# Optimization experiments

Hardware: AMD Instinct MI355X
Metric: run time of the kernel (lower is better)

## Reference

```python
import jax, jax.numpy as jnp
import numpy as np

B, X, T = 4, 128, 256
PARAM_DIM, HIDDEN, EMB, DH, LATENT = 16, 128, 128, 32, 32


def _w(key, fan_in, fan_out):
    return jax.random.normal(key, (fan_in, fan_out), dtype=jnp.float32) / np.sqrt(fan_in)


def setup_inputs() -> dict:
    key = jax.random.key(0)
    ks = jax.random.split(key, 32)
    d = {
        "x": jax.random.normal(ks[0], (B, X, 1), dtype=jnp.float32),
        "t": jax.random.normal(ks[1], (B, T, 1), dtype=jnp.float32),
        "param": jax.random.normal(ks[2], (B, PARAM_DIM), dtype=jnp.float32),
        # p2e: SymmetricInitDNN([param_dim, hidden, emb], 'sin')
        "p2e_W1": _w(ks[3], PARAM_DIM, HIDDEN), "p2e_b1": jnp.zeros((HIDDEN,), jnp.float32),
        "p2e_W2": _w(ks[4], HIDDEN, EMB), "p2e_b2": jnp.zeros((EMB,), jnp.float32),
        "e2ex_W": _w(ks[5], EMB, EMB), "e2ex_b": jnp.zeros((EMB,), jnp.float32),
        "e2et_W": _w(ks[6], EMB, EMB), "e2et_b": jnp.zeros((EMB,), jnp.float32),
        # PX for x: sin-MLP on coord, FiLM-modulated by embedding, learned mult
        "px_Wx": _w(ks[7], 1, HIDDEN), "px_bx": jnp.zeros((HIDDEN,), jnp.float32),
        "px_We": _w(ks[8], EMB, HIDDEN), "px_be": jnp.zeros((HIDDEN,), jnp.float32),
        "px_Wo": _w(ks[9], HIDDEN, DH * LATENT), "px_bo": jnp.zeros((DH * LATENT,), jnp.float32),
        "px_mult": jnp.ones((), jnp.float32),
        # PX for t
        "zt_Wx": _w(ks[10], 1, HIDDEN), "zt_bx": jnp.zeros((HIDDEN,), jnp.float32),
        "zt_We": _w(ks[11], EMB, HIDDEN), "zt_be": jnp.zeros((HIDDEN,), jnp.float32),
        "zt_Wo": _w(ks[12], HIDDEN, DH * LATENT), "zt_bo": jnp.zeros((DH * LATENT,), jnp.float32),
        "zt_mult": jnp.ones((), jnp.float32),
        "h0": jnp.zeros((1, HIDDEN), jnp.float32),
        # BlockMod(dh, hidden, 'sin'): conditioned residual block (num_blocks=1)
        "blk_W1": _w(ks[13], HIDDEN, HIDDEN), "blk_b1": jnp.zeros((HIDDEN,), jnp.float32),
        "blk_Wc": _w(ks[14], DH, HIDDEN), "blk_bc": jnp.zeros((HIDDEN,), jnp.float32),
        "blk_W2": _w(ks[15], HIDDEN, HIDDEN), "blk_b2": jnp.zeros((HIDDEN,), jnp.float32),
        # d: SymmetricInitDNN([hidden, 1], 'identity') -> single linear
        "d_W": _w(ks[16], HIDDEN, 1), "d_b": jnp.zeros((1,), jnp.float32),
    }
    return d


def reference(x, t, param,
              p2e_W1, p2e_b1, p2e_W2, p2e_b2,
              e2ex_W, e2ex_b, e2et_W, e2et_b,
              px_Wx, px_bx, px_We, px_be, px_Wo, px_bo, px_mult,
              zt_Wx, zt_bx, zt_We, zt_be, zt_Wo, zt_bo, zt_mult,
              h0, blk_W1, blk_b1, blk_Wc, blk_bc, blk_W2, blk_b2,
              d_W, d_b):
    # param embedding: sin-MLP then two linear heads
    e = jnp.sin(param @ p2e_W1 + p2e_b1) @ p2e_W2 + p2e_b2          # (B, EMB)
    ex = e @ e2ex_W + e2ex_b                                        # (B, EMB)
    et = e @ e2et_W + e2et_b                                        # (B, EMB)

    # PX(x, ex): sin feature of coord FiLM-modulated by embedding
    fx = jnp.sin(x @ px_Wx + px_bx) * (ex @ px_We + px_be)[:, None, :]
    px = px_mult * (fx @ px_Wo + px_bo)                             # (B, X, DH*LATENT)
    px = px.reshape(px.shape[0], px.shape[1], DH, LATENT)           # (B, X, DH, LATENT)

    ft = jnp.sin(t @ zt_Wx + zt_bx) * (et @ zt_We + zt_be)[:, None, :]
    zt = zt_mult * (ft @ zt_Wo + zt_bo)                             # (B, T, DH*LATENT)
    zt = zt.reshape(zt.shape[0], zt.shape[1], DH, LATENT)           # (B, T, DH, LATENT)

    # mean over latent of broadcast outer product: (B, T, X, DH)
    ztpx = jnp.einsum('btdl,bxdl->btxd', zt, px) / LATENT

    # h0 broadcast to (B, T, X, HIDDEN)
    h = jnp.broadcast_to(h0[:, None, None, :], ztpx.shape[:3] + (HIDDEN,))
    # BlockMod: conditioned residual block (sin activation)
    h = h + (jnp.sin(h @ blk_W1 + blk_b1) * (ztpx @ blk_Wc + blk_bc)) @ blk_W2 + blk_b2

    u_pred = h @ d_W + d_b                                          # (B, T, X, 1)
    return u_pred, zt, px
```

## Files before the change

### kernel.cpp

```cpp
#include <hip/hip_runtime.h>
#include <math.h>


typedef __attribute__((ext_vector_type(8))) short short8v;
typedef __attribute__((ext_vector_type(4))) float f32x4;

struct P {
    const float *x, *t, *param;
    const float *p2e_W1, *p2e_b1, *p2e_W2, *p2e_b2;
    const float *e2ex_W, *e2ex_b, *e2et_W, *e2et_b;
    const float *px_Wx, *px_bx, *px_We, *px_be, *px_Wo, *px_bo, *px_mult;
    const float *zt_Wx, *zt_bx, *zt_We, *zt_be, *zt_Wo, *zt_bo, *zt_mult;
    const float *h0, *blk_W1, *blk_b1, *blk_Wc, *blk_bc, *blk_W2, *blk_b2;
    const float *d_W, *d_b;
    float *out_u, *out_zt, *out_px, *ws;
    unsigned short *ztbf_g, *pxbf_g;
};

__device__ __forceinline__ void fma4(float4& a, float s, const float4& v) {
    a.x += s * v.x; a.y += s * v.y; a.z += s * v.z; a.w += s * v.w;
}

__device__ __forceinline__ unsigned short f2bf(float f) {
    unsigned int u = __float_as_uint(f);
    return (unsigned short)((u + 0x7FFFu + ((u >> 16) & 1u)) >> 16);
}

__device__ __forceinline__ void gemv_stage(
    const float* __restrict__ W, const float* __restrict__ bias,
    const float* vin, float* vout, float* partf, int tid)
{
    const int j4 = tid & 31;
    const int sl = tid >> 5;
    float4 a4 = make_float4(0.f, 0.f, 0.f, 0.f);
    const float* Wp = W + sl * 16 * 128 + j4 * 4;
    #pragma unroll
    for (int k = 0; k < 16; ++k)
        fma4(a4, vin[sl * 16 + k], *(const float4*)&Wp[k * 128]);
    *(float4*)&partf[sl * 128 + j4 * 4] = a4;
    __syncthreads();
    if (tid < 128) {
        float v = bias[tid];
        #pragma unroll
        for (int q = 0; q < 8; ++q) v += partf[q * 128 + tid];
        vout[tid] = v;
    }
    __syncthreads();
}

__global__ __launch_bounds__(256, 2) void feat_kernel(P p) {
    __shared__ float vin[128], vout[128];
    __shared__ float partf[1024];
    __shared__ unsigned short fbf[32 * 136];
    __shared__ unsigned short wot[128 * 136];
    const int tid = threadIdx.x;
    const int bid = blockIdx.x;

    if (bid < 384) {
        const bool is_zt = bid >= 128;
        int b, rt, cq;
        if (!is_zt) { b = bid >> 5;          rt = (bid >> 3) & 3;          cq = bid & 7; }
        else        { const int un = bid - 128; b = un >> 6; rt = (un >> 3) & 7; cq = un & 7; }
        const int R   = is_zt ? 256 : 128;
        const int r0g = b * R + rt * 32;
        const int co0 = cq * 128;

        const float* Wh = is_zt ? p.e2et_W : p.e2ex_W;
        const float* bh = is_zt ? p.e2et_b : p.e2ex_b;
        const float* We = is_zt ? p.zt_We : p.px_We;
        const float* be = is_zt ? p.zt_be : p.px_be;
        const float* Wx = is_zt ? p.zt_Wx : p.px_Wx;
        const float* bxv = is_zt ? p.zt_bx : p.px_bx;
        const float* Wo = is_zt ? p.zt_Wo : p.px_Wo;
        const float* bo = is_zt ? p.zt_bo : p.px_bo;
        const float* coord = is_zt ? p.t : p.x;
        const float mult = is_zt ? p.zt_mult[0] : p.px_mult[0];
        float* outp = is_zt ? p.out_zt : p.out_px;
        unsigned short* obf = is_zt ? p.ztbf_g : p.pxbf_g;

        if (tid < 128) {
            float a = p.p2e_b1[tid];
            #pragma unroll
            for (int q = 0; q < 16; ++q)
                a += p.param[b * 16 + q] * p.p2e_W1[q * 128 + tid];
            vin[tid] = __sinf(a);
        }
        __syncthreads();
        gemv_stage(p.p2e_W2, p.p2e_b2, vin, vout, partf, tid);
        gemv_stage(Wh, bh, vout, vin, partf, tid);
        gemv_stage(We, be, vin, vout, partf, tid);

        {
            const int j  = tid & 127;
            const int rh = tid >> 7;
            const float g = vout[j];
            const float wxj = Wx[j], bxj = bxv[j];
            #pragma unroll
            for (int rr = 0; rr < 16; ++rr) {
                const int row = rh * 16 + rr;
                fbf[row * 136 + j] =
                    f2bf(__sinf(coord[r0g + row] * wxj + bxj) * g);
            }
        }

        #pragma unroll
        for (int i = 0; i < 2; ++i) {
            const int s  = tid + 256 * i;
            const int kt = s >> 5;
            const int ct = s & 31;
            float4 r[8];
            #pragma unroll
            for (int kk = 0; kk < 8; ++kk)
                r[kk] = *(const float4*)&Wo[(kt * 8 + kk) * 1024 + co0 + ct * 4];
            #pragma unroll
            for (int c = 0; c < 4; ++c) {
                short8v o;
                #pragma unroll
                for (int kk = 0; kk < 8; ++kk)
                    o[kk] = (short)f2bf(((const float*)&r[kk])[c]);
                *(short8v*)&wot[(ct * 4 + c) * 136 + kt * 8] = o;
            }
        }
        __syncthreads();

        const int l   = tid & 63;
        const int wid = tid >> 6;
        f32x4 a00 = {0.f,0.f,0.f,0.f}, a01 = {0.f,0.f,0.f,0.f};
        f32x4 a10 = {0.f,0.f,0.f,0.f}, a11 = {0.f,0.f,0.f,0.f};
        const int rsel = (l & 15) * 136;
        #pragma unroll
        for (int ks = 0; ks < 4; ++ks) {
            const int koff = ks * 32 + (l >> 4) * 8;
            const short8v fa0 = *(const short8v*)&fbf[rsel + koff];
            const short8v fa1 = *(const short8v*)&fbf[16 * 136 + rsel + koff];
            const short8v wb0 = *(const short8v*)&wot[(wid * 32) * 136 + rsel + koff];
            const short8v wb1 = *(const short8v*)&wot[(wid * 32 + 16) * 136 + rsel + koff];
            a00 = __builtin_amdgcn_mfma_f32_16x16x32_bf16(fa0, wb0, a00, 0, 0, 0);
            a01 = __builtin_amdgcn_mfma_f32_16x16x32_bf16(fa0, wb1, a01, 0, 0, 0);
            a10 = __builtin_amdgcn_mfma_f32_16x16x32_bf16(fa1, wb0, a10, 0, 0, 0);
            a11 = __builtin_amdgcn_mfma_f32_16x16x32_bf16(fa1, wb1, a11, 0, 0, 0);
        }

        const int crow = (l >> 4) * 4;
        const int ccol = l & 15;
        const int cb   = co0 + wid * 32 + ccol;
        const float b0v = bo[cb];
        const float b1v = bo[cb + 16];
        #pragma unroll
        for (int r = 0; r < 4; ++r) {
            const int ra = (r0g + crow + r) * 1024;
            const int rb = (r0g + 16 + crow + r) * 1024;
            const float v00 = mult * (a00[r] + b0v);
            const float v01 = mult * (a01[r] + b1v);
            const float v10 = mult * (a10[r] + b0v);
            const float v11 = mult * (a11[r] + b1v);
            outp[ra + cb]      = v00;
            outp[ra + cb + 16] = v01;
            outp[rb + cb]      = v10;
            outp[rb + cb + 16] = v11;
            if (obf) {
                obf[ra + cb]      = f2bf(v00);
                obf[ra + cb + 16] = f2bf(v01);
                obf[rb + cb]      = f2bf(v10);
                obf[rb + cb + 16] = f2bf(v11);
            }
        }
    } else {
        __shared__ float dws[128];
        if (tid < 128) { vin[tid] = p.h0[tid]; dws[tid] = p.d_W[tid]; }
        __syncthreads();
        gemv_stage(p.blk_W1, p.blk_b1, vin, vout, partf, tid);
        if (tid < 128) {
            float w2 = 0.f;
            const float4* rp = (const float4*)&p.blk_W2[tid * 128];
            #pragma unroll
            for (int m4 = 0; m4 < 32; ++m4) {
                const float4 wv = rp[m4];
                const float4 dv = *(const float4*)&dws[m4 * 4];
                w2 += wv.x * dv.x + wv.y * dv.y + wv.z * dv.z + wv.w * dv.w;
            }
            const float sv = __sinf(vout[tid]) * w2;
            vin[tid] = sv;
            vout[tid] = (p.h0[tid] + p.blk_b2[tid]) * dws[tid] + sv * p.blk_bc[tid];
        }
        __syncthreads();
        {
            const int d  = tid >> 3;
            const int sg = (tid & 7) * 16;
            float acc = 0.f;
            #pragma unroll
            for (int i4 = 0; i4 < 4; ++i4) {
                const float4 wv = *(const float4*)&p.blk_Wc[d * 128 + sg + i4 * 4];
                const float4 sv = *(const float4*)&vin[sg + i4 * 4];
                acc += wv.x * sv.x + wv.y * sv.y + wv.z * sv.z + wv.w * sv.w;
            }
            partf[d * 8 + (tid & 7)] = acc;
        }
        __syncthreads();
        if (tid < 32) {
            float w = 0.f;
            #pragma unroll
            for (int q = 0; q < 8; ++q) w += partf[tid * 8 + q];
            p.ws[tid] = w * (1.0f / 32.0f);
        }
        if (tid < 64) vout[tid] += vout[tid + 64];
        __syncthreads();
        if (tid == 0) {
            float K = p.d_b[0];
            #pragma unroll
            for (int i = 0; i < 64; ++i) K += vout[i];
            p.ws[32] = K;
        }
    }
}

__global__ __launch_bounds__(256) void u_bf_kernel(
    const unsigned short* __restrict__ ztg, const unsigned short* __restrict__ pxg,
    const float* __restrict__ ws, float* __restrict__ out_u)
{
    __shared__ unsigned short ztbf[16 * 536];
    __shared__ unsigned short pxbf[32 * 536];
    __shared__ float red[4 * 2 * 256];
    __shared__ float wcs[32];
    __shared__ float K0s;

    const int tid = threadIdx.x;
    const int bid = blockIdx.x;
    const int b   = bid >> 6;
    const int rem = bid & 63;
    const int t0  = (rem >> 2) * 16;
    const int x0  = (rem & 3) * 32;

    if (tid < 32) wcs[tid] = ws[tid];
    if (tid == 32) K0s = ws[32];

    const unsigned short* ztb = ztg + (b * 256 + t0) * 1024;
    const unsigned short* pxb = pxg + (b * 128 + x0) * 1024;
    const int l   = tid & 63;
    const int wid = tid >> 6;

    f32x4 acc0 = {0.f, 0.f, 0.f, 0.f};
    f32x4 acc1 = {0.f, 0.f, 0.f, 0.f};

    __syncthreads();

    for (int h = 0; h < 2; ++h) {
        const int kb = h * 512;
        if (h) __syncthreads();

        #pragma unroll
        for (int i = 0; i < 4; ++i) {
            const int s   = tid + 256 * i;
            const int row = s >> 6;
            const int kc8 = (s & 63) * 8;
            *(short8v*)&ztbf[row * 536 + kc8] =
                *(const short8v*)&ztb[row * 1024 + kb + kc8];
        }
        #pragma unroll
        for (int i = 0; i < 8; ++i) {
            const int s   = tid + 256 * i;
            const int row = s >> 6;
            const int kc8 = (s & 63) * 8;
            *(short8v*)&pxbf[row * 536 + kc8] =
                *(const short8v*)&pxb[row * 1024 + kb + kc8];
        }
        __syncthreads();

        const int rsel = (l & 15) * 536;
        #pragma unroll
        for (int ks = 0; ks < 4; ++ks) {
            const int kloc = wid * 128 + ks * 32 + (l >> 4) * 8;
            const float w = wcs[h * 16 + wid * 4 + ks];
            const short8v a  = *(const short8v*)&ztbf[rsel + kloc];
            const short8v b0 = *(const short8v*)&pxbf[rsel + kloc];
            const short8v b1 = *(const short8v*)&pxbf[rsel + 16 * 536 + kloc];
            const f32x4 z = {0.f, 0.f, 0.f, 0.f};
            const f32x4 t0v = __builtin_amdgcn_mfma_f32_16x16x32_bf16(a, b0, z, 0, 0, 0);
            const f32x4 t1v = __builtin_amdgcn_mfma_f32_16x16x32_bf16(a, b1, z, 0, 0, 0);
            #pragma unroll
            for (int r = 0; r < 4; ++r) {
                acc0[r] += w * t0v[r];
                acc1[r] += w * t1v[r];
            }
        }
    }

    #pragma unroll
    for (int r = 0; r < 4; ++r) {
        red[(wid * 2 + 0) * 256 + l * 4 + r] = acc0[r];
        red[(wid * 2 + 1) * 256 + l * 4 + r] = acc1[r];
    }
    __syncthreads();

    {
        const int ll = tid & 63;
        const int rr = tid >> 6;
        const int ri = ll * 4 + rr;
        const int tt = t0 + ((ll >> 4) << 2) + rr;
        #pragma unroll
        for (int xt = 0; xt < 2; ++xt) {
            float sum = K0s;
            #pragma unroll
            for (int w = 0; w < 4; ++w) sum += red[(w * 2 + xt) * 256 + ri];
            const int xx = x0 + xt * 16 + (ll & 15);
            out_u[(b * 256 + tt) * 128 + xx] = sum;
        }
    }
}

__global__ __launch_bounds__(256) void u_kernel(
    const float* __restrict__ zt, const float* __restrict__ px,
    const float* __restrict__ ws, float* __restrict__ out_u)
{
    __shared__ unsigned short ztbf[16 * 536];
    __shared__ unsigned short pxbf[32 * 536];
    __shared__ float red[4 * 2 * 256];
    __shared__ float wcs[32];
    __shared__ float K0s;

    const int tid = threadIdx.x;
    const int bid = blockIdx.x;
    const int b   = bid >> 6;
    const int rem = bid & 63;
    const int t0  = (rem >> 2) * 16;
    const int x0  = (rem & 3) * 32;

    if (tid < 32) wcs[tid] = ws[tid];
    if (tid == 32) K0s = ws[32];

    const float* ztb = zt + (b * 256 + t0) * 1024;
    const float* pxb = px + (b * 128 + x0) * 1024;
    const int l   = tid & 63;
    const int wid = tid >> 6;

    f32x4 acc0 = {0.f, 0.f, 0.f, 0.f};
    f32x4 acc1 = {0.f, 0.f, 0.f, 0.f};

    __syncthreads();

    for (int h = 0; h < 2; ++h) {
        const int kb = h * 512;
        if (h) __syncthreads();

        #pragma unroll
        for (int i = 0; i < 4; ++i) {
            const int s   = tid + 256 * i;
            const int row = s >> 6;
            const int kc8 = (s & 63) * 8;
            const float* src = ztb + row * 1024 + kb + kc8;
            const float4 v0 = *(const float4*)src;
            const float4 v1 = *(const float4*)(src + 4);
            short8v o;
            o[0] = (short)f2bf(v0.x); o[1] = (short)f2bf(v0.y);
            o[2] = (short)f2bf(v0.z); o[3] = (short)f2bf(v0.w);
            o[4] = (short)f2bf(v1.x); o[5] = (short)f2bf(v1.y);
            o[6] = (short)f2bf(v1.z); o[7] = (short)f2bf(v1.w);
            *(short8v*)&ztbf[row * 536 + kc8] = o;
        }
        #pragma unroll
        for (int i = 0; i < 8; ++i) {
            const int s   = tid + 256 * i;
            const int row = s >> 6;
            const int kc8 = (s & 63) * 8;
            const float sc = wcs[(kb + kc8) >> 5];
            const float* src = pxb + row * 1024 + kb + kc8;
            const float4 v0 = *(const float4*)src;
            const float4 v1 = *(const float4*)(src + 4);
            short8v o;
            o[0] = (short)f2bf(sc * v0.x); o[1] = (short)f2bf(sc * v0.y);
            o[2] = (short)f2bf(sc * v0.z); o[3] = (short)f2bf(sc * v0.w);
            o[4] = (short)f2bf(sc * v1.x); o[5] = (short)f2bf(sc * v1.y);
            o[6] = (short)f2bf(sc * v1.z); o[7] = (short)f2bf(sc * v1.w);
            *(short8v*)&pxbf[row * 536 + kc8] = o;
        }
        __syncthreads();

        const int rsel = (l & 15) * 536;
        #pragma unroll
        for (int ks = 0; ks < 4; ++ks) {
            const int kloc = wid * 128 + ks * 32 + (l >> 4) * 8;
            const short8v a  = *(const short8v*)&ztbf[rsel + kloc];
            const short8v b0 = *(const short8v*)&pxbf[rsel + kloc];
            const short8v b1 = *(const short8v*)&pxbf[rsel + 16 * 536 + kloc];
            acc0 = __builtin_amdgcn_mfma_f32_16x16x32_bf16(a, b0, acc0, 0, 0, 0);
            acc1 = __builtin_amdgcn_mfma_f32_16x16x32_bf16(a, b1, acc1, 0, 0, 0);
        }
    }

    #pragma unroll
    for (int r = 0; r < 4; ++r) {
        red[(wid * 2 + 0) * 256 + l * 4 + r] = acc0[r];
        red[(wid * 2 + 1) * 256 + l * 4 + r] = acc1[r];
    }
    __syncthreads();

    {
        const int ll = tid & 63;
        const int rr = tid >> 6;
        const int ri = ll * 4 + rr;
        const int tt = t0 + ((ll >> 4) << 2) + rr;
        #pragma unroll
        for (int xt = 0; xt < 2; ++xt) {
            float sum = K0s;
            #pragma unroll
            for (int w = 0; w < 4; ++w) sum += red[(w * 2 + xt) * 256 + ri];
            const int xx = x0 + xt * 16 + (ll & 15);
            out_u[(b * 256 + tt) * 128 + xx] = sum;
        }
    }
}

extern "C" void kernel_launch(void* const* d_in, const int* in_sizes, int n_in,
                              void* d_out, int out_size, void* d_ws, size_t ws_size,
                              hipStream_t stream) {
    float* out = (float*)d_out;
    float* ws  = (float*)d_ws;

    const size_t need = 64 * sizeof(float) + (size_t)(1048576 + 524288) * 2 + 4096;
    const bool use_bf = ws_size >= need;
    unsigned short* ztbf_g = use_bf ? (unsigned short*)(ws + 64) : nullptr;
    unsigned short* pxbf_g = use_bf ? (unsigned short*)(ws + 64) + 1048576 : nullptr;

    P prm;
    prm.x       = (const float*)d_in[0];
    prm.t       = (const float*)d_in[1];
    prm.param   = (const float*)d_in[2];
    prm.p2e_W1  = (const float*)d_in[3];
    prm.p2e_b1  = (const float*)d_in[4];
    prm.p2e_W2  = (const float*)d_in[5];
    prm.p2e_b2  = (const float*)d_in[6];
    prm.e2ex_W  = (const float*)d_in[7];
    prm.e2ex_b  = (const float*)d_in[8];
    prm.e2et_W  = (const float*)d_in[9];
    prm.e2et_b  = (const float*)d_in[10];
    prm.px_Wx   = (const float*)d_in[11];
    prm.px_bx   = (const float*)d_in[12];
    prm.px_We   = (const float*)d_in[13];
    prm.px_be   = (const float*)d_in[14];
    prm.px_Wo   = (const float*)d_in[15];
    prm.px_bo   = (const float*)d_in[16];
    prm.px_mult = (const float*)d_in[17];
    prm.zt_Wx   = (const float*)d_in[18];
    prm.zt_bx   = (const float*)d_in[19];
    prm.zt_We   = (const float*)d_in[20];
    prm.zt_be   = (const float*)d_in[21];
    prm.zt_Wo   = (const float*)d_in[22];
    prm.zt_bo   = (const float*)d_in[23];
    prm.zt_mult = (const float*)d_in[24];
    prm.h0      = (const float*)d_in[25];
    prm.blk_W1  = (const float*)d_in[26];
    prm.blk_b1  = (const float*)d_in[27];
    prm.blk_Wc  = (const float*)d_in[28];
    prm.blk_bc  = (const float*)d_in[29];
    prm.blk_W2  = (const float*)d_in[30];
    prm.blk_b2  = (const float*)d_in[31];
    prm.d_W     = (const float*)d_in[32];
    prm.d_b     = (const float*)d_in[33];
    prm.out_u   = out;
    prm.out_zt  = out + 131072;
    prm.out_px  = out + 131072 + 1048576;
    prm.ws      = ws;
    prm.ztbf_g  = ztbf_g;
    prm.pxbf_g  = pxbf_g;

    feat_kernel<<<385, 256, 0, stream>>>(prm);
    if (use_bf)
        u_bf_kernel<<<256, 256, 0, stream>>>(ztbf_g, pxbf_g, ws, out);
    else
        u_kernel<<<256, 256, 0, stream>>>(prm.out_zt, prm.out_px, ws, out);
}
```

Baseline: 19.81 us.

## Double row tiles per block in feature and u kernels, halving grid sizes

The feature kernel now handles 64 rows per block instead of 32, so each block reuses its staged bf16 Wo tile across four MFMA row tiles. This halves the number of blocks that each recompute the embedding GEMV chain and convert Wo. The u_bf kernel now covers a 32x32 (t,x) tile with K split into four 256-wide chunks, so every staged zt and px row serves two MFMA tiles. Fewer blocks (193 and 128) on a chip with many CUs lowers parallelism and occupancy, and the longer per-block serial work may offset the reduced redundant work.

```diff
diff --git a/kernel.cpp b/kernel.cpp
--- a/kernel.cpp
+++ b/kernel.cpp
@@ -51,18 +51,18 @@
 __global__ __launch_bounds__(256, 2) void feat_kernel(P p) {
     __shared__ float vin[128], vout[128];
     __shared__ float partf[1024];
-    __shared__ unsigned short fbf[32 * 136];
+    __shared__ unsigned short fbf[64 * 136];
     __shared__ unsigned short wot[128 * 136];
     const int tid = threadIdx.x;
     const int bid = blockIdx.x;
 
-    if (bid < 384) {
-        const bool is_zt = bid >= 128;
+    if (bid < 192) {
+        const bool is_zt = bid >= 64;
         int b, rt, cq;
-        if (!is_zt) { b = bid >> 5;          rt = (bid >> 3) & 3;          cq = bid & 7; }
-        else        { const int un = bid - 128; b = un >> 6; rt = (un >> 3) & 7; cq = un & 7; }
+        if (!is_zt) { b = bid >> 4;           rt = (bid >> 3) & 1; cq = bid & 7; }
+        else        { const int un = bid - 64; b = un >> 5; rt = (un >> 3) & 3; cq = un & 7; }
         const int R   = is_zt ? 256 : 128;
-        const int r0g = b * R + rt * 32;
+        const int r0g = b * R + rt * 64;
         const int co0 = cq * 128;
 
         const float* Wh = is_zt ? p.e2et_W : p.e2ex_W;
@@ -96,8 +96,8 @@
             const float g = vout[j];
             const float wxj = Wx[j], bxj = bxv[j];
             #pragma unroll
-            for (int rr = 0; rr < 16; ++rr) {
-                const int row = rh * 16 + rr;
+            for (int rr = 0; rr < 32; ++rr) {
+                const int row = rh * 32 + rr;
                 fbf[row * 136 + j] =
                     f2bf(__sinf(coord[r0g + row] * wxj + bxj) * g);
             }
@@ -125,20 +125,24 @@
 
         const int l   = tid & 63;
         const int wid = tid >> 6;
-        f32x4 a00 = {0.f,0.f,0.f,0.f}, a01 = {0.f,0.f,0.f,0.f};
-        f32x4 a10 = {0.f,0.f,0.f,0.f}, a11 = {0.f,0.f,0.f,0.f};
+        f32x4 acc[4][2];
+        #pragma unroll
+        for (int tt = 0; tt < 4; ++tt)
+            #pragma unroll
+            for (int ct = 0; ct < 2; ++ct)
+                acc[tt][ct] = (f32x4){0.f, 0.f, 0.f, 0.f};
         const int rsel = (l & 15) * 136;
         #pragma unroll
         for (int ks = 0; ks < 4; ++ks) {
             const int koff = ks * 32 + (l >> 4) * 8;
-            const short8v fa0 = *(const short8v*)&fbf[rsel + koff];
-            const short8v fa1 = *(const short8v*)&fbf[16 * 136 + rsel + koff];
             const short8v wb0 = *(const short8v*)&wot[(wid * 32) * 136 + rsel + koff];
             const short8v wb1 = *(const short8v*)&wot[(wid * 32 + 16) * 136 + rsel + koff];
-            a00 = __builtin_amdgcn_mfma_f32_16x16x32_bf16(fa0, wb0, a00, 0, 0, 0);
-            a01 = __builtin_amdgcn_mfma_f32_16x16x32_bf16(fa0, wb1, a01, 0, 0, 0);
-            a10 = __builtin_amdgcn_mfma_f32_16x16x32_bf16(fa1, wb0, a10, 0, 0, 0);
-            a11 = __builtin_amdgcn_mfma_f32_16x16x32_bf16(fa1, wb1, a11, 0, 0, 0);
+            #pragma unroll
+            for (int tt = 0; tt < 4; ++tt) {
+                const short8v fa = *(const short8v*)&fbf[(tt * 16) * 136 + rsel + koff];
+                acc[tt][0] = __builtin_amdgcn_mfma_f32_16x16x32_bf16(fa, wb0, acc[tt][0], 0, 0, 0);
+                acc[tt][1] = __builtin_amdgcn_mfma_f32_16x16x32_bf16(fa, wb1, acc[tt][1], 0, 0, 0);
+            }
         }
 
         const int crow = (l >> 4) * 4;
@@ -147,22 +151,18 @@
         const float b0v = bo[cb];
         const float b1v = bo[cb + 16];
         #pragma unroll
-        for (int r = 0; r < 4; ++r) {
-            const int ra = (r0g + crow + r) * 1024;
-            const int rb = (r0g + 16 + crow + r) * 1024;
-            const float v00 = mult * (a00[r] + b0v);
-            const float v01 = mult * (a01[r] + b1v);
-            const float v10 = mult * (a10[r] + b0v);
-            const float v11 = mult * (a11[r] + b1v);
-            outp[ra + cb]      = v00;
-            outp[ra + cb + 16] = v01;
-            outp[rb + cb]      = v10;
-            outp[rb + cb + 16] = v11;
-            if (obf) {
-                obf[ra + cb]      = f2bf(v00);
-                obf[ra + cb + 16] = f2bf(v01);
-                obf[rb + cb]      = f2bf(v10);
-                obf[rb + cb + 16] = f2bf(v11);
+        for (int tt = 0; tt < 4; ++tt) {
+            #pragma unroll
+            for (int r = 0; r < 4; ++r) {
+                const int ro = (r0g + tt * 16 + crow + r) * 1024;
+                const float v0 = mult * (acc[tt][0][r] + b0v);
+                const float v1 = mult * (acc[tt][1][r] + b1v);
+                outp[ro + cb]      = v0;
+                outp[ro + cb + 16] = v1;
+                if (obf) {
+                    obf[ro + cb]      = f2bf(v0);
+                    obf[ro + cb + 16] = f2bf(v1);
+                }
             }
         }
     } else {
@@ -218,17 +218,17 @@
     const unsigned short* __restrict__ ztg, const unsigned short* __restrict__ pxg,
     const float* __restrict__ ws, float* __restrict__ out_u)
 {
-    __shared__ unsigned short ztbf[16 * 536];
-    __shared__ unsigned short pxbf[32 * 536];
-    __shared__ float red[4 * 2 * 256];
+    __shared__ unsigned short ztbf[32 * 264];
+    __shared__ unsigned short pxbf[32 * 264];
+    __shared__ float red[16 * 256];
     __shared__ float wcs[32];
     __shared__ float K0s;
 
     const int tid = threadIdx.x;
     const int bid = blockIdx.x;
-    const int b   = bid >> 6;
-    const int rem = bid & 63;
-    const int t0  = (rem >> 2) * 16;
+    const int b   = bid >> 5;
+    const int rem = bid & 31;
+    const int t0  = (rem >> 2) * 32;
     const int x0  = (rem & 3) * 32;
 
     if (tid < 32) wcs[tid] = ws[tid];
@@ -239,71 +239,86 @@
     const int l   = tid & 63;
     const int wid = tid >> 6;
 
-    f32x4 acc0 = {0.f, 0.f, 0.f, 0.f};
-    f32x4 acc1 = {0.f, 0.f, 0.f, 0.f};
-
-    __syncthreads();
-
-    for (int h = 0; h < 2; ++h) {
-        const int kb = h * 512;
-        if (h) __syncthreads();
+    f32x4 acc[2][2];
+    #pragma unroll
+    for (int it = 0; it < 2; ++it)
+        #pragma unroll
+        for (int ix = 0; ix < 2; ++ix)
+            acc[it][ix] = (f32x4){0.f, 0.f, 0.f, 0.f};
+
+    __syncthreads();
+
+    for (int q = 0; q < 4; ++q) {
+        const int kb = q * 256;
+        if (q) __syncthreads();
 
         #pragma unroll
         for (int i = 0; i < 4; ++i) {
             const int s   = tid + 256 * i;
-            const int row = s >> 6;
-            const int kc8 = (s & 63) * 8;
-            *(short8v*)&ztbf[row * 536 + kc8] =
+            const int row = s >> 5;
+            const int kc8 = (s & 31) * 8;
+            *(short8v*)&ztbf[row * 264 + kc8] =
                 *(const short8v*)&ztb[row * 1024 + kb + kc8];
         }
         #pragma unroll
-        for (int i = 0; i < 8; ++i) {
+        for (int i = 0; i < 4; ++i) {
             const int s   = tid + 256 * i;
-            const int row = s >> 6;
-            const int kc8 = (s & 63) * 8;
-            *(short8v*)&pxbf[row * 536 + kc8] =
+            const int row = s >> 5;
+            const int kc8 = (s & 31) * 8;
+            *(short8v*)&pxbf[row * 264 + kc8] =
                 *(const short8v*)&pxb[row * 1024 + kb + kc8];
         }
         __syncthreads();
 
-        const int rsel = (l & 15) * 536;
-        #pragma unroll
-        for (int ks = 0; ks < 4; ++ks) {
-            const int kloc = wid * 128 + ks * 32 + (l >> 4) * 8;
-            const float w = wcs[h * 16 + wid * 4 + ks];
-            const short8v a  = *(const short8v*)&ztbf[rsel + kloc];
+        const int rsel = (l & 15) * 264;
+        #pragma unroll
+        for (int ks = 0; ks < 2; ++ks) {
+            const int kloc = wid * 64 + ks * 32 + (l >> 4) * 8;
+            const float w = wcs[q * 8 + wid * 2 + ks];
+            const short8v a0 = *(const short8v*)&ztbf[rsel + kloc];
+            const short8v a1 = *(const short8v*)&ztbf[16 * 264 + rsel + kloc];
             const short8v b0 = *(const short8v*)&pxbf[rsel + kloc];
-            const short8v b1 = *(const short8v*)&pxbf[rsel + 16 * 536 + kloc];
+            const short8v b1 = *(const short8v*)&pxbf[16 * 264 + rsel + kloc];
             const f32x4 z = {0.f, 0.f, 0.f, 0.f};
-            const f32x4 t0v = __builtin_amdgcn_mfma_f32_16x16x32_bf16(a, b0, z, 0, 0, 0);
-            const f32x4 t1v = __builtin_amdgcn_mfma_f32_16x16x32_bf16(a, b1, z, 0, 0, 0);
+            const f32x4 t00 = __builtin_amdgcn_mfma_f32_16x16x32_bf16(a0, b0, z, 0, 0, 0);
+            const f32x4 t01 = __builtin_amdgcn_mfma_f32_16x16x32_bf16(a0, b1, z, 0, 0, 0);
+            const f32x4 t10 = __builtin_amdgcn_mfma_f32_16x16x32_bf16(a1, b0, z, 0, 0, 0);
+            const f32x4 t11 = __builtin_amdgcn_mfma_f32_16x16x32_bf16(a1, b1, z, 0, 0, 0);
             #pragma unroll
             for (int r = 0; r < 4; ++r) {
-                acc0[r] += w * t0v[r];
-                acc1[r] += w * t1v[r];
+                acc[0][0][r] += w * t00[r];
+                acc[0][1][r] += w * t01[r];
+                acc[1][0][r] += w * t10[r];
+                acc[1][1][r] += w * t11[r];
             }
         }
     }
 
     #pragma unroll
-    for (int r = 0; r < 4; ++r) {
-        red[(wid * 2 + 0) * 256 + l * 4 + r] = acc0[r];
-        red[(wid * 2 + 1) * 256 + l * 4 + r] = acc1[r];
-    }
+    for (int it = 0; it < 2; ++it)
+        #pragma unroll
+        for (int ix = 0; ix < 2; ++ix)
+            #pragma unroll
+            for (int r = 0; r < 4; ++r)
+                red[(wid * 4 + it * 2 + ix) * 256 + l * 4 + r] = acc[it][ix][r];
     __syncthreads();
 
     {
         const int ll = tid & 63;
         const int rr = tid >> 6;
         const int ri = ll * 4 + rr;
-        const int tt = t0 + ((ll >> 4) << 2) + rr;
-        #pragma unroll
-        for (int xt = 0; xt < 2; ++xt) {
-            float sum = K0s;
-            #pragma unroll
-            for (int w = 0; w < 4; ++w) sum += red[(w * 2 + xt) * 256 + ri];
-            const int xx = x0 + xt * 16 + (ll & 15);
-            out_u[(b * 256 + tt) * 128 + xx] = sum;
+        const int trow = ((ll >> 4) << 2) + rr;
+        const int col  = ll & 15;
+        #pragma unroll
+        for (int it = 0; it < 2; ++it) {
+            #pragma unroll
+            for (int ix = 0; ix < 2; ++ix) {
+                float sum = K0s;
+                #pragma unroll
+                for (int w = 0; w < 4; ++w)
+                    sum += red[(w * 4 + it * 2 + ix) * 256 + ri];
+                out_u[(b * 256 + t0 + it * 16 + trow) * 128 + x0 + ix * 16 + col] = sum;
+            }
         }
     }
 }
@@ -463,9 +478,9 @@
     prm.ztbf_g  = ztbf_g;
     prm.pxbf_g  = pxbf_g;
 
-    feat_kernel<<<385, 256, 0, stream>>>(prm);
+    feat_kernel<<<193, 256, 0, stream>>>(prm);
     if (use_bf)
-        u_bf_kernel<<<256, 256, 0, stream>>>(ztbf_g, pxbf_g, ws, out);
+        u_bf_kernel<<<128, 256, 0, stream>>>(ztbf_g, pxbf_g, ws, out);
     else
         u_kernel<<<256, 256, 0, stream>>>(prm.out_zt, prm.out_px, ws, out);
 }
```

Result: slower. 26.27 us (+32.7%).
